# Kernel tuning notes

Measured on AMD Instinct MI355X. Metric: run time of the kernel, lower is better.

## Reference

```python
import jax, jax.numpy as jnp
import numpy as np

HEADS = 8
HEAD_DIM = 32
PRE_H = 32
PRE_W = 32
SCALE = HEAD_DIM ** (-0.5)


def _relative_indices(H, W):
    # Faithful to torch loop: out[p, q] = (gy[q]-y_p+H)*W + (gx[q]-x_p+W)
    gy, gx = np.meshgrid(np.arange(H), np.arange(W), indexing='ij')
    gy = gy.reshape(-1)
    gx = gx.reshape(-1)
    idx = (gy[None, :] - gy[:, None] + H) * W + (gx[None, :] - gx[:, None] + W)
    return idx.astype(np.int32)  # [HW, HW]


def setup_inputs() -> dict:
    key = jax.random.key(0)
    ks = jax.random.split(key, 7)
    b, c, H, W = 16, 256, PRE_H, PRE_W
    dim = HEADS * HEAD_DIM  # 256
    x = jax.random.normal(ks[0], (b, c, H, W), dtype=jnp.float32)
    # nn.Linear weights: [out_features, in_features]
    Wq = jax.random.normal(ks[1], (dim, c), dtype=jnp.float32) * 0.02
    Wk = jax.random.normal(ks[2], (dim, c), dtype=jnp.float32) * 0.02
    Wv = jax.random.normal(ks[3], (dim, c), dtype=jnp.float32) * 0.02
    Wo = jax.random.normal(ks[4], (c, dim), dtype=jnp.float32) * 0.02
    bo = jax.random.normal(ks[5], (c,), dtype=jnp.float32) * 0.02
    rel_bias = jax.random.normal(ks[6], (HEADS, (2 * PRE_H - 1) * (2 * PRE_W - 1)), dtype=jnp.float32)
    rel_idx = jnp.asarray(_relative_indices(PRE_H, PRE_W))
    return {"x": x, "Wq": Wq, "Wk": Wk, "Wv": Wv, "Wo": Wo, "bo": bo,
            "rel_bias": rel_bias, "rel_idx": rel_idx}


def reference(x, Wq, Wk, Wv, Wo, bo, rel_bias, rel_idx):
    b, c, H, W = x.shape
    n = H * W
    h, d = HEADS, HEAD_DIM
    # b c h w -> b (h w) c
    xt = x.reshape(b, c, n).transpose(0, 2, 1)
    q = (xt @ Wq.T).reshape(b, n, h, d).transpose(0, 2, 1, 3)  # b h n d
    k = (xt @ Wk.T).reshape(b, n, h, d).transpose(0, 2, 1, 3)
    v = (xt @ Wv.T).reshape(b, n, h, d).transpose(0, 2, 1, 3)
    k = k * SCALE
    # gathered relative bias: [h, n, n]
    bias = rel_bias[:, rel_idx]
    attn = jnp.einsum('bhnd,bhmd->bhnm', q, k) + bias[None]
    attn = jax.nn.softmax(attn, axis=-1)
    out = jnp.einsum('bhnm,bhmd->bhnd', attn, v)
    out = out.transpose(0, 2, 1, 3).reshape(b, n, h * d)  # b n (h d)
    out = out @ Wo.T + bo
    # b (h w) c -> b c h w
    return out.transpose(0, 2, 1).reshape(b, c, H, W)
```

## Files before the change

### kernel.cpp

```cpp
#include <hip/hip_runtime.h>

#define HEADS 8
#define HDIM 32
#define NTOK 1024
#define CDIM 256
#define BATCH 16
#define ATT_SCALE 0.17677669529663687f
#define L2E 1.4426950408889634f
#define VSTR 1032

typedef __attribute__((ext_vector_type(8))) short bf16x8;
typedef __attribute__((ext_vector_type(4))) float f32x4;

__device__ __forceinline__ unsigned short f2bf(float f) {
    unsigned int u = __float_as_uint(f);
    return (unsigned short)((u + 0x7fffu + ((u >> 16) & 1u)) >> 16);
}

__global__ __launch_bounds__(256) void prep_kernel(
    const float* __restrict__ x,
    const float* __restrict__ Wq, const float* __restrict__ Wk,
    const float* __restrict__ Wv, const float* __restrict__ Wo,
    unsigned short* __restrict__ w16, unsigned short* __restrict__ xt16)
{
    const int t = threadIdx.x;
    if (blockIdx.z == 16) {
        const int which = blockIdx.y;
        const float* src = (which == 0) ? Wq : ((which == 1) ? Wk : ((which == 2) ? Wv : Wo));
        const float scale = (which == 1) ? (ATT_SCALE * L2E) : 1.0f;
        const int base = (blockIdx.x * 256 + t) * 16;
        #pragma unroll
        for (int i = 0; i < 4; ++i) {
            const int idx = base + i * 4;
            float4 v = *(const float4*)&src[idx];
            union { unsigned short h[4]; uint2 u; } pk;
            pk.h[0] = f2bf(v.x * scale); pk.h[1] = f2bf(v.y * scale);
            pk.h[2] = f2bf(v.z * scale); pk.h[3] = f2bf(v.w * scale);
            *(uint2*)&w16[(size_t)which * 65536 + idx] = pk.u;
        }
        return;
    }
    __shared__ float tile[64][65];
    const int b = blockIdx.z, ct = blockIdx.y * 64, nt = blockIdx.x * 64;
    const float* xb = x + ((size_t)b * CDIM + ct) * NTOK + nt;
    const int cc = t >> 4, n4 = (t & 15) * 4;
    #pragma unroll
    for (int i = 0; i < 4; ++i) {
        float4 v = *(const float4*)&xb[(size_t)(cc + 16 * i) * NTOK + n4];
        tile[cc + 16 * i][n4]     = v.x;
        tile[cc + 16 * i][n4 + 1] = v.y;
        tile[cc + 16 * i][n4 + 2] = v.z;
        tile[cc + 16 * i][n4 + 3] = v.w;
    }
    __syncthreads();
    const int c0 = (t & 15) * 4;
    #pragma unroll
    for (int i = 0; i < 4; ++i) {
        const int nl = (t >> 4) + 16 * i;
        union { unsigned short h[4]; uint2 u; } pk;
        #pragma unroll
        for (int j = 0; j < 4; ++j) pk.h[j] = f2bf(tile[c0 + j][nl]);
        *(uint2*)&xt16[((size_t)b * NTOK + nt + nl) * CDIM + ct + c0] = pk.u;
    }
}

__global__ __launch_bounds__(1024, 4) void attn_kernel(
    const unsigned short* __restrict__ xt16,
    const unsigned short* __restrict__ w16,
    const float* __restrict__ rel_bias,
    unsigned short* __restrict__ ao16)
{
    __shared__ __align__(16) unsigned char smem[65536 + VSTR * 32 * 2 + 2080 * 4];
    unsigned short* k_s  = (unsigned short*)smem;
    unsigned short* v_s  = (unsigned short*)(smem + 65536);
    unsigned short* q_s  = (unsigned short*)(smem + 65536);
    float*          bias_s = (float*)(smem + 65536 + VSTR * 32 * 2);

    const int id   = blockIdx.x;
    const int bh_i = (id & 7) * 16 + (id >> 4);
    const int half = (id >> 3) & 1;
    const int b = bh_i >> 3, h = bh_i & 7;

    const int t = threadIdx.x, wid = t >> 6, lane = t & 63;
    const int g = lane >> 4, ln = lane & 15;
    const int qb = half * 512 + wid * 32;

    const unsigned short* xb  = xt16 + (size_t)b * NTOK * CDIM;
    const unsigned short* wqh = w16 + (size_t)(h * 32) * CDIM;
    const unsigned short* wkh = w16 + 65536 + (size_t)(h * 32) * CDIM;
    const unsigned short* wvh = w16 + 2 * 65536 + (size_t)(h * 32) * CDIM;

    {
        const float* brow = rel_bias + (size_t)h * 3969;
        for (int i = t; i < 2080; i += 1024) bias_s[i] = brow[i] * L2E;
    }

    {
        const int tr = wid * 64;
        f32x4 acc[4][2];
        #pragma unroll
        for (int m = 0; m < 4; ++m)
            #pragma unroll
            for (int n = 0; n < 2; ++n) acc[m][n] = (f32x4){0.f, 0.f, 0.f, 0.f};
        for (int kt = 0; kt < CDIM; kt += 32) {
            bf16x8 a[4], w2[2];
            #pragma unroll
            for (int m = 0; m < 4; ++m)
                a[m] = *(const bf16x8*)&xb[(size_t)(tr + m * 16 + ln) * CDIM + kt + g * 8];
            #pragma unroll
            for (int n = 0; n < 2; ++n)
                w2[n] = *(const bf16x8*)&wkh[(size_t)(n * 16 + ln) * CDIM + kt + g * 8];
            #pragma unroll
            for (int m = 0; m < 4; ++m)
                #pragma unroll
                for (int n = 0; n < 2; ++n)
                    acc[m][n] = __builtin_amdgcn_mfma_f32_16x16x32_bf16(a[m], w2[n], acc[m][n], 0, 0, 0);
        }
        #pragma unroll
        for (int m = 0; m < 4; ++m)
            #pragma unroll
            for (int n = 0; n < 2; ++n)
                #pragma unroll
                for (int r = 0; r < 4; ++r)
                    k_s[(size_t)(tr + m * 16 + g * 4 + r) * HDIM + n * 16 + ln] = f2bf(acc[m][n][r]);
    }

    bf16x8 aq0, aq1;
    {
        f32x4 acc[2][2];
        #pragma unroll
        for (int m = 0; m < 2; ++m)
            #pragma unroll
            for (int n = 0; n < 2; ++n) acc[m][n] = (f32x4){0.f, 0.f, 0.f, 0.f};
        for (int kt = 0; kt < CDIM; kt += 32) {
            bf16x8 a[2], w2[2];
            #pragma unroll
            for (int m = 0; m < 2; ++m)
                a[m] = *(const bf16x8*)&xb[(size_t)(qb + m * 16 + ln) * CDIM + kt + g * 8];
            #pragma unroll
            for (int n = 0; n < 2; ++n)
                w2[n] = *(const bf16x8*)&wqh[(size_t)(n * 16 + ln) * CDIM + kt + g * 8];
            #pragma unroll
            for (int m = 0; m < 2; ++m)
                #pragma unroll
                for (int n = 0; n < 2; ++n)
                    acc[m][n] = __builtin_amdgcn_mfma_f32_16x16x32_bf16(a[m], w2[n], acc[m][n], 0, 0, 0);
        }
        const int lr = wid * 32;
        #pragma unroll
        for (int m = 0; m < 2; ++m)
            #pragma unroll
            for (int n = 0; n < 2; ++n)
                #pragma unroll
                for (int r = 0; r < 4; ++r)
                    q_s[(size_t)(lr + m * 16 + g * 4 + r) * HDIM + n * 16 + ln] = f2bf(acc[m][n][r]);
        aq0 = *(const bf16x8*)&q_s[(size_t)(lr + ln) * HDIM + g * 8];
        aq1 = *(const bf16x8*)&q_s[(size_t)(lr + 16 + ln) * HDIM + g * 8];
    }

    __syncthreads();

    {
        const int tb = wid * 64;
        f32x4 acc[2][4];
        #pragma unroll
        for (int m = 0; m < 2; ++m)
            #pragma unroll
            for (int n = 0; n < 4; ++n) acc[m][n] = (f32x4){0.f, 0.f, 0.f, 0.f};
        for (int kt = 0; kt < CDIM; kt += 32) {
            bf16x8 aw[2], bx[4];
            #pragma unroll
            for (int m = 0; m < 2; ++m)
                aw[m] = *(const bf16x8*)&wvh[(size_t)(m * 16 + ln) * CDIM + kt + g * 8];
            #pragma unroll
            for (int n = 0; n < 4; ++n)
                bx[n] = *(const bf16x8*)&xb[(size_t)(tb + n * 16 + ln) * CDIM + kt + g * 8];
            #pragma unroll
            for (int m = 0; m < 2; ++m)
                #pragma unroll
                for (int n = 0; n < 4; ++n)
                    acc[m][n] = __builtin_amdgcn_mfma_f32_16x16x32_bf16(aw[m], bx[n], acc[m][n], 0, 0, 0);
        }
        #pragma unroll
        for (int m = 0; m < 2; ++m)
            #pragma unroll
            for (int n = 0; n < 4; ++n)
                #pragma unroll
                for (int r = 0; r < 4; ++r)
                    v_s[(size_t)(m * 16 + g * 4 + r) * VSTR + tb + n * 16 + ln] = f2bf(acc[m][n][r]);
    }

    __syncthreads();

    const int jrow  = 8 * (ln >> 2) + (ln & 3);
    const int boff0 = 1056 + 8 * g - qb - ln;
    const int boff1 = boff0 - 16;

    f32x4 o00 = {0.f,0.f,0.f,0.f}, o01 = {0.f,0.f,0.f,0.f};
    f32x4 o10 = {0.f,0.f,0.f,0.f}, o11 = {0.f,0.f,0.f,0.f};
    f32x4 ls0 = {0.f,0.f,0.f,0.f}, ls1 = {0.f,0.f,0.f,0.f};
    const short one_bf = (short)0x3F80;
    const bf16x8 ones = {one_bf,one_bf,one_bf,one_bf,one_bf,one_bf,one_bf,one_bf};

    for (int kb = 0; kb < NTOK; kb += 32) {
        const bf16x8 kf0 = *(const bf16x8*)&k_s[(size_t)(kb + jrow) * HDIM + g * 8];
        const bf16x8 kf1 = *(const bf16x8*)&k_s[(size_t)(kb + jrow + 4) * HDIM + g * 8];
        const bf16x8 vA0 = *(const bf16x8*)&v_s[(size_t)ln * VSTR + kb + g * 8];
        const bf16x8 vA1 = *(const bf16x8*)&v_s[(size_t)(16 + ln) * VSTR + kb + g * 8];
        float bc0[8], bc1[8];
        #pragma unroll
        for (int i = 0; i < 8; ++i) bc0[i] = bias_s[kb + boff0 + i];
        #pragma unroll
        for (int i = 0; i < 8; ++i) bc1[i] = bias_s[kb + boff1 + i];

        f32x4 s00 = __builtin_amdgcn_mfma_f32_16x16x32_bf16(kf0, aq0, (f32x4){0.f,0.f,0.f,0.f}, 0, 0, 0);
        f32x4 s01 = __builtin_amdgcn_mfma_f32_16x16x32_bf16(kf1, aq0, (f32x4){0.f,0.f,0.f,0.f}, 0, 0, 0);
        f32x4 s10 = __builtin_amdgcn_mfma_f32_16x16x32_bf16(kf0, aq1, (f32x4){0.f,0.f,0.f,0.f}, 0, 0, 0);
        f32x4 s11 = __builtin_amdgcn_mfma_f32_16x16x32_bf16(kf1, aq1, (f32x4){0.f,0.f,0.f,0.f}, 0, 0, 0);

        union { int i4[4]; bf16x8 v; } ap0, ap1;
        #pragma unroll
        for (int r = 0; r < 4; ++r) {
            float e0 = __builtin_amdgcn_exp2f(s00[r] + bc0[r]);
            float e1 = __builtin_amdgcn_exp2f(s01[r] + bc0[4 + r]);
            unsigned u0 = __float_as_uint(e0) + 0x8000u;
            unsigned u1 = __float_as_uint(e1) + 0x8000u;
            ((unsigned short*)ap0.i4)[r]     = (unsigned short)(u0 >> 16);
            ((unsigned short*)ap0.i4)[4 + r] = (unsigned short)(u1 >> 16);
        }
        #pragma unroll
        for (int r = 0; r < 4; ++r) {
            float e0 = __builtin_amdgcn_exp2f(s10[r] + bc1[r]);
            float e1 = __builtin_amdgcn_exp2f(s11[r] + bc1[4 + r]);
            unsigned u0 = __float_as_uint(e0) + 0x8000u;
            unsigned u1 = __float_as_uint(e1) + 0x8000u;
            ((unsigned short*)ap1.i4)[r]     = (unsigned short)(u0 >> 16);
            ((unsigned short*)ap1.i4)[4 + r] = (unsigned short)(u1 >> 16);
        }

        o00 = __builtin_amdgcn_mfma_f32_16x16x32_bf16(ap0.v, vA0, o00, 0, 0, 0);
        o01 = __builtin_amdgcn_mfma_f32_16x16x32_bf16(ap0.v, vA1, o01, 0, 0, 0);
        ls0 = __builtin_amdgcn_mfma_f32_16x16x32_bf16(ap0.v, ones, ls0, 0, 0, 0);
        o10 = __builtin_amdgcn_mfma_f32_16x16x32_bf16(ap1.v, vA0, o10, 0, 0, 0);
        o11 = __builtin_amdgcn_mfma_f32_16x16x32_bf16(ap1.v, vA1, o11, 0, 0, 0);
        ls1 = __builtin_amdgcn_mfma_f32_16x16x32_bf16(ap1.v, ones, ls1, 0, 0, 0);
    }

    #pragma unroll
    for (int r = 0; r < 4; ++r) {
        float i0 = 1.f / ls0[r], i1 = 1.f / ls1[r];
        o00[r] *= i0; o01[r] *= i0;
        o10[r] *= i1; o11[r] *= i1;
    }

    __syncthreads();
    unsigned short (*otr)[32][40] = (unsigned short(*)[32][40])smem;
    #pragma unroll
    for (int r = 0; r < 4; ++r) {
        otr[wid][g * 4 + r][ln]           = f2bf(o00[r]);
        otr[wid][g * 4 + r][16 + ln]      = f2bf(o01[r]);
        otr[wid][16 + g * 4 + r][ln]      = f2bf(o10[r]);
        otr[wid][16 + g * 4 + r][16 + ln] = f2bf(o11[r]);
    }
    const int row = lane >> 1;
    const int ch  = (lane & 1) * 16;
    uint4 st0 = *(uint4*)&otr[wid][row][ch];
    uint4 st1 = *(uint4*)&otr[wid][row][ch + 8];
    unsigned short* dst = &ao16[((size_t)b * NTOK + qb + row) * CDIM + h * HDIM + ch];
    *(uint4*)dst     = st0;
    *(uint4*)&dst[8] = st1;
}

__global__ __launch_bounds__(256) void outproj_kernel(
    const unsigned short* __restrict__ ao16,
    const unsigned short* __restrict__ wo16,
    const float* __restrict__ bo,
    float* __restrict__ y)
{
    const int id   = blockIdx.x;
    const int b    = (id & 7) * 2 + ((id >> 3) & 1);
    const int rest = id >> 4;
    const int ct   = (rest & 3) * 64;
    const int pt   = (rest >> 2) * 64;
    const int t = threadIdx.x, wid = t >> 6, lane = t & 63;
    const int g = lane >> 4, ln = lane & 15;
    const int cbase = ct + wid * 16;
    const unsigned short* ab = ao16 + (size_t)b * NTOK * CDIM;
    f32x4 acc[4];
    #pragma unroll
    for (int i = 0; i < 4; ++i) acc[i] = (f32x4){0.f, 0.f, 0.f, 0.f};

    for (int kt = 0; kt < CDIM; kt += 32) {
        bf16x8 aw = *(const bf16x8*)&wo16[(size_t)(cbase + ln) * CDIM + kt + g * 8];
        #pragma unroll
        for (int t2 = 0; t2 < 4; ++t2) {
            bf16x8 bx = *(const bf16x8*)&ab[(size_t)(pt + t2 * 16 + ln) * CDIM + kt + g * 8];
            acc[t2] = __builtin_amdgcn_mfma_f32_16x16x32_bf16(aw, bx, acc[t2], 0, 0, 0);
        }
    }
    #pragma unroll
    for (int r = 0; r < 4; ++r) {
        const int c = cbase + g * 4 + r;
        const float bias = bo[c];
        #pragma unroll
        for (int t2 = 0; t2 < 4; ++t2)
            y[((size_t)b * CDIM + c) * NTOK + pt + t2 * 16 + ln] = acc[t2][r] + bias;
    }
}

extern "C" void kernel_launch(void* const* d_in, const int* in_sizes, int n_in,
                              void* d_out, int out_size, void* d_ws, size_t ws_size,
                              hipStream_t stream) {
    const float* x        = (const float*)d_in[0];
    const float* Wq       = (const float*)d_in[1];
    const float* Wk       = (const float*)d_in[2];
    const float* Wv       = (const float*)d_in[3];
    const float* Wo       = (const float*)d_in[4];
    const float* bo       = (const float*)d_in[5];
    const float* rel_bias = (const float*)d_in[6];
    (void)in_sizes; (void)n_in; (void)ws_size; (void)out_size;

    unsigned short* ws16 = (unsigned short*)d_ws;
    unsigned short* xt16 = ws16;
    unsigned short* ao16 = ws16 + (size_t)4 * 1024 * 1024;
    unsigned short* w16  = ws16 + (size_t)8 * 1024 * 1024;
    float* y = (float*)d_out;

    prep_kernel<<<dim3(16, 4, 17), 256, 0, stream>>>(x, Wq, Wk, Wv, Wo, w16, xt16);
    attn_kernel<<<256, 1024, 0, stream>>>(xt16, w16, rel_bias, ao16);
    outproj_kernel<<<1024, 256, 0, stream>>>(ao16, w16 + 3 * 65536, bo, y);
}
```

Measured before the change: 189.3 us.

## Fuse K/V projections, swizzle K smem, seed scores with bias, retile outproj

Computes the K and V projections in one loop so each x fragment is loaded once for both. The K tile in shared memory gets an XOR swizzle to reduce bank conflicts. The relative bias is stored as four shifted copies, so each lane loads it as aligned float4 vectors and feeds it as the MFMA accumulator init, which removes the separate bias adds. The exp-to-bf16 packing is simplified, and the output projection is retiled to 128-token blocks with 2x4 MFMA tiles per wave, halving the grid. Costs are more shared memory for the bias copies and higher register pressure from the fused accumulators and full unrolling.

```diff
diff --git a/kernel.cpp b/kernel.cpp
--- a/kernel.cpp
+++ b/kernel.cpp
@@ -8,6 +8,7 @@
 #define ATT_SCALE 0.17677669529663687f
 #define L2E 1.4426950408889634f
 #define VSTR 1032
+#define BSTR 1540
 
 typedef __attribute__((ext_vector_type(8))) short bf16x8;
 typedef __attribute__((ext_vector_type(4))) float f32x4;
@@ -16,6 +17,8 @@
     unsigned int u = __float_as_uint(f);
     return (unsigned short)((u + 0x7fffu + ((u >> 16) & 1u)) >> 16);
 }
+
+__device__ __forceinline__ int kswz(int row) { return (row + (row >> 3)) & 3; }
 
 __global__ __launch_bounds__(256) void prep_kernel(
     const float* __restrict__ x,
@@ -70,11 +73,11 @@
     const float* __restrict__ rel_bias,
     unsigned short* __restrict__ ao16)
 {
-    __shared__ __align__(16) unsigned char smem[65536 + VSTR * 32 * 2 + 2080 * 4];
-    unsigned short* k_s  = (unsigned short*)smem;
-    unsigned short* v_s  = (unsigned short*)(smem + 65536);
-    unsigned short* q_s  = (unsigned short*)(smem + 65536);
-    float*          bias_s = (float*)(smem + 65536 + VSTR * 32 * 2);
+    __shared__ __align__(16) unsigned char smem[65536 + VSTR * 32 * 2 + BSTR * 4 * 4];
+    unsigned short* k_s   = (unsigned short*)smem;
+    unsigned short* v_s   = (unsigned short*)(smem + 65536);
+    unsigned short* q_s   = (unsigned short*)(smem + 65536);
+    float*          bias4 = (float*)(smem + 65536 + VSTR * 32 * 2);
 
     const int id   = blockIdx.x;
     const int bh_i = (id & 7) * 16 + (id >> 4);
@@ -91,38 +94,13 @@
     const unsigned short* wvh = w16 + 2 * 65536 + (size_t)(h * 32) * CDIM;
 
     {
+        const int START = 544 - 512 * half;
         const float* brow = rel_bias + (size_t)h * 3969;
-        for (int i = t; i < 2080; i += 1024) bias_s[i] = brow[i] * L2E;
-    }
-
-    {
-        const int tr = wid * 64;
-        f32x4 acc[4][2];
-        #pragma unroll
-        for (int m = 0; m < 4; ++m)
-            #pragma unroll
-            for (int n = 0; n < 2; ++n) acc[m][n] = (f32x4){0.f, 0.f, 0.f, 0.f};
-        for (int kt = 0; kt < CDIM; kt += 32) {
-            bf16x8 a[4], w2[2];
-            #pragma unroll
-            for (int m = 0; m < 4; ++m)
-                a[m] = *(const bf16x8*)&xb[(size_t)(tr + m * 16 + ln) * CDIM + kt + g * 8];
-            #pragma unroll
-            for (int n = 0; n < 2; ++n)
-                w2[n] = *(const bf16x8*)&wkh[(size_t)(n * 16 + ln) * CDIM + kt + g * 8];
-            #pragma unroll
-            for (int m = 0; m < 4; ++m)
-                #pragma unroll
-                for (int n = 0; n < 2; ++n)
-                    acc[m][n] = __builtin_amdgcn_mfma_f32_16x16x32_bf16(a[m], w2[n], acc[m][n], 0, 0, 0);
-        }
-        #pragma unroll
-        for (int m = 0; m < 4; ++m)
-            #pragma unroll
-            for (int n = 0; n < 2; ++n)
-                #pragma unroll
-                for (int r = 0; r < 4; ++r)
-                    k_s[(size_t)(tr + m * 16 + g * 4 + r) * HDIM + n * 16 + ln] = f2bf(acc[m][n][r]);
+        for (int i = t; i < 1540; i += 1024) {
+            #pragma unroll
+            for (int a = 0; a < 4; ++a)
+                bias4[a * BSTR + i] = brow[START + a + i] * L2E;
+        }
     }
 
     bf16x8 aq0, aq1;
@@ -132,6 +110,7 @@
         for (int m = 0; m < 2; ++m)
             #pragma unroll
             for (int n = 0; n < 2; ++n) acc[m][n] = (f32x4){0.f, 0.f, 0.f, 0.f};
+        #pragma unroll
         for (int kt = 0; kt < CDIM; kt += 32) {
             bf16x8 a[2], w2[2];
             #pragma unroll
@@ -161,40 +140,64 @@
     __syncthreads();
 
     {
-        const int tb = wid * 64;
-        f32x4 acc[2][4];
-        #pragma unroll
-        for (int m = 0; m < 2; ++m)
-            #pragma unroll
-            for (int n = 0; n < 4; ++n) acc[m][n] = (f32x4){0.f, 0.f, 0.f, 0.f};
+        const int tr = wid * 64;
+        f32x4 ak[4][2], av[2][4];
+        #pragma unroll
+        for (int m = 0; m < 4; ++m)
+            #pragma unroll
+            for (int n = 0; n < 2; ++n) {
+                ak[m][n] = (f32x4){0.f, 0.f, 0.f, 0.f};
+                av[n][m] = (f32x4){0.f, 0.f, 0.f, 0.f};
+            }
+        #pragma unroll
         for (int kt = 0; kt < CDIM; kt += 32) {
-            bf16x8 aw[2], bx[4];
-            #pragma unroll
-            for (int m = 0; m < 2; ++m)
-                aw[m] = *(const bf16x8*)&wvh[(size_t)(m * 16 + ln) * CDIM + kt + g * 8];
-            #pragma unroll
-            for (int n = 0; n < 4; ++n)
-                bx[n] = *(const bf16x8*)&xb[(size_t)(tb + n * 16 + ln) * CDIM + kt + g * 8];
-            #pragma unroll
-            for (int m = 0; m < 2; ++m)
+            bf16x8 xf[4], wkf[2], wvf[2];
+            #pragma unroll
+            for (int m = 0; m < 4; ++m)
+                xf[m] = *(const bf16x8*)&xb[(size_t)(tr + m * 16 + ln) * CDIM + kt + g * 8];
+            #pragma unroll
+            for (int n = 0; n < 2; ++n) {
+                wkf[n] = *(const bf16x8*)&wkh[(size_t)(n * 16 + ln) * CDIM + kt + g * 8];
+                wvf[n] = *(const bf16x8*)&wvh[(size_t)(n * 16 + ln) * CDIM + kt + g * 8];
+            }
+            #pragma unroll
+            for (int m = 0; m < 4; ++m) {
+                ak[m][0] = __builtin_amdgcn_mfma_f32_16x16x32_bf16(xf[m], wkf[0], ak[m][0], 0, 0, 0);
+                ak[m][1] = __builtin_amdgcn_mfma_f32_16x16x32_bf16(xf[m], wkf[1], ak[m][1], 0, 0, 0);
+                av[0][m] = __builtin_amdgcn_mfma_f32_16x16x32_bf16(wvf[0], xf[m], av[0][m], 0, 0, 0);
+                av[1][m] = __builtin_amdgcn_mfma_f32_16x16x32_bf16(wvf[1], xf[m], av[1][m], 0, 0, 0);
+            }
+        }
+        #pragma unroll
+        for (int m = 0; m < 4; ++m)
+            #pragma unroll
+            for (int n = 0; n < 2; ++n)
                 #pragma unroll
-                for (int n = 0; n < 4; ++n)
-                    acc[m][n] = __builtin_amdgcn_mfma_f32_16x16x32_bf16(aw[m], bx[n], acc[m][n], 0, 0, 0);
-        }
-        #pragma unroll
-        for (int m = 0; m < 2; ++m)
-            #pragma unroll
-            for (int n = 0; n < 4; ++n)
+                for (int r = 0; r < 4; ++r) {
+                    const int row = tr + m * 16 + g * 4 + r;
+                    const int col = n * 16 + ln;
+                    k_s[row * 32 + (((col >> 3) ^ kswz(row)) << 3) + (col & 7)] = f2bf(ak[m][n][r]);
+                }
+        #pragma unroll
+        for (int n = 0; n < 2; ++n)
+            #pragma unroll
+            for (int m = 0; m < 4; ++m)
                 #pragma unroll
                 for (int r = 0; r < 4; ++r)
-                    v_s[(size_t)(m * 16 + g * 4 + r) * VSTR + tb + n * 16 + ln] = f2bf(acc[m][n][r]);
+                    v_s[(size_t)(n * 16 + g * 4 + r) * VSTR + tr + m * 16 + ln] = f2bf(av[n][m][r]);
     }
 
     __syncthreads();
 
-    const int jrow  = 8 * (ln >> 2) + (ln & 3);
-    const int boff0 = 1056 + 8 * g - qb - ln;
-    const int boff1 = boff0 - 16;
+    const int jrow = 8 * (ln >> 2) + (ln & 3);
+    const int jr1  = jrow + 4;
+    const int koff0 = jrow * 32 + ((g ^ kswz(jrow)) << 3);
+    const int koff1 = jr1 * 32 + ((g ^ kswz(jr1)) << 3);
+    const int boffL = 512 + 8 * g - wid * 32 - ln;
+    const int ba = boffL & 3;
+    const float* bb = &bias4[ba * BSTR + (boffL - ba)];
+    const unsigned short* vr0 = &v_s[(size_t)ln * VSTR + g * 8];
+    const unsigned short* vr1 = &v_s[(size_t)(16 + ln) * VSTR + g * 8];
 
     f32x4 o00 = {0.f,0.f,0.f,0.f}, o01 = {0.f,0.f,0.f,0.f};
     f32x4 o10 = {0.f,0.f,0.f,0.f}, o11 = {0.f,0.f,0.f,0.f};
@@ -203,39 +206,38 @@
     const bf16x8 ones = {one_bf,one_bf,one_bf,one_bf,one_bf,one_bf,one_bf,one_bf};
 
     for (int kb = 0; kb < NTOK; kb += 32) {
-        const bf16x8 kf0 = *(const bf16x8*)&k_s[(size_t)(kb + jrow) * HDIM + g * 8];
-        const bf16x8 kf1 = *(const bf16x8*)&k_s[(size_t)(kb + jrow + 4) * HDIM + g * 8];
-        const bf16x8 vA0 = *(const bf16x8*)&v_s[(size_t)ln * VSTR + kb + g * 8];
-        const bf16x8 vA1 = *(const bf16x8*)&v_s[(size_t)(16 + ln) * VSTR + kb + g * 8];
-        float bc0[8], bc1[8];
-        #pragma unroll
-        for (int i = 0; i < 8; ++i) bc0[i] = bias_s[kb + boff0 + i];
-        #pragma unroll
-        for (int i = 0; i < 8; ++i) bc1[i] = bias_s[kb + boff1 + i];
-
-        f32x4 s00 = __builtin_amdgcn_mfma_f32_16x16x32_bf16(kf0, aq0, (f32x4){0.f,0.f,0.f,0.f}, 0, 0, 0);
-        f32x4 s01 = __builtin_amdgcn_mfma_f32_16x16x32_bf16(kf1, aq0, (f32x4){0.f,0.f,0.f,0.f}, 0, 0, 0);
-        f32x4 s10 = __builtin_amdgcn_mfma_f32_16x16x32_bf16(kf0, aq1, (f32x4){0.f,0.f,0.f,0.f}, 0, 0, 0);
-        f32x4 s11 = __builtin_amdgcn_mfma_f32_16x16x32_bf16(kf1, aq1, (f32x4){0.f,0.f,0.f,0.f}, 0, 0, 0);
-
-        union { int i4[4]; bf16x8 v; } ap0, ap1;
-        #pragma unroll
-        for (int r = 0; r < 4; ++r) {
-            float e0 = __builtin_amdgcn_exp2f(s00[r] + bc0[r]);
-            float e1 = __builtin_amdgcn_exp2f(s01[r] + bc0[4 + r]);
-            unsigned u0 = __float_as_uint(e0) + 0x8000u;
-            unsigned u1 = __float_as_uint(e1) + 0x8000u;
-            ((unsigned short*)ap0.i4)[r]     = (unsigned short)(u0 >> 16);
-            ((unsigned short*)ap0.i4)[4 + r] = (unsigned short)(u1 >> 16);
-        }
-        #pragma unroll
-        for (int r = 0; r < 4; ++r) {
-            float e0 = __builtin_amdgcn_exp2f(s10[r] + bc1[r]);
-            float e1 = __builtin_amdgcn_exp2f(s11[r] + bc1[4 + r]);
-            unsigned u0 = __float_as_uint(e0) + 0x8000u;
-            unsigned u1 = __float_as_uint(e1) + 0x8000u;
-            ((unsigned short*)ap1.i4)[r]     = (unsigned short)(u0 >> 16);
-            ((unsigned short*)ap1.i4)[4 + r] = (unsigned short)(u1 >> 16);
+        const bf16x8 kf0 = *(const bf16x8*)&k_s[kb * 32 + koff0];
+        const bf16x8 kf1 = *(const bf16x8*)&k_s[kb * 32 + koff1];
+        const bf16x8 vA0 = *(const bf16x8*)&vr0[kb];
+        const bf16x8 vA1 = *(const bf16x8*)&vr1[kb];
+        const f32x4 cA0 = *(const f32x4*)&bb[kb];
+        const f32x4 cA1 = *(const f32x4*)&bb[kb + 4];
+        const f32x4 cB0 = *(const f32x4*)&bb[kb - 16];
+        const f32x4 cB1 = *(const f32x4*)&bb[kb - 12];
+
+        f32x4 s00 = __builtin_amdgcn_mfma_f32_16x16x32_bf16(kf0, aq0, cA0, 0, 0, 0);
+        f32x4 s01 = __builtin_amdgcn_mfma_f32_16x16x32_bf16(kf1, aq0, cA1, 0, 0, 0);
+        f32x4 s10 = __builtin_amdgcn_mfma_f32_16x16x32_bf16(kf0, aq1, cB0, 0, 0, 0);
+        f32x4 s11 = __builtin_amdgcn_mfma_f32_16x16x32_bf16(kf1, aq1, cB1, 0, 0, 0);
+
+        union { unsigned u4[4]; bf16x8 v; } ap0, ap1;
+        #pragma unroll
+        for (int p2 = 0; p2 < 2; ++p2) {
+            unsigned ua = __float_as_uint(__builtin_amdgcn_exp2f(s00[2 * p2]))     + 0x8000u;
+            unsigned ub = __float_as_uint(__builtin_amdgcn_exp2f(s00[2 * p2 + 1])) + 0x8000u;
+            ap0.u4[p2]     = (ub & 0xffff0000u) | (ua >> 16);
+            unsigned uc = __float_as_uint(__builtin_amdgcn_exp2f(s01[2 * p2]))     + 0x8000u;
+            unsigned ud = __float_as_uint(__builtin_amdgcn_exp2f(s01[2 * p2 + 1])) + 0x8000u;
+            ap0.u4[2 + p2] = (ud & 0xffff0000u) | (uc >> 16);
+        }
+        #pragma unroll
+        for (int p2 = 0; p2 < 2; ++p2) {
+            unsigned ua = __float_as_uint(__builtin_amdgcn_exp2f(s10[2 * p2]))     + 0x8000u;
+            unsigned ub = __float_as_uint(__builtin_amdgcn_exp2f(s10[2 * p2 + 1])) + 0x8000u;
+            ap1.u4[p2]     = (ub & 0xffff0000u) | (ua >> 16);
+            unsigned uc = __float_as_uint(__builtin_amdgcn_exp2f(s11[2 * p2]))     + 0x8000u;
+            unsigned ud = __float_as_uint(__builtin_amdgcn_exp2f(s11[2 * p2 + 1])) + 0x8000u;
+            ap1.u4[2 + p2] = (ud & 0xffff0000u) | (uc >> 16);
         }
 
         o00 = __builtin_amdgcn_mfma_f32_16x16x32_bf16(ap0.v, vA0, o00, 0, 0, 0);
@@ -281,31 +283,44 @@
     const int b    = (id & 7) * 2 + ((id >> 3) & 1);
     const int rest = id >> 4;
     const int ct   = (rest & 3) * 64;
-    const int pt   = (rest >> 2) * 64;
+    const int pt   = (rest >> 2) * 128;
     const int t = threadIdx.x, wid = t >> 6, lane = t & 63;
     const int g = lane >> 4, ln = lane & 15;
-    const int cbase = ct + wid * 16;
+    const int cb2 = ct + (wid & 1) * 32;
+    const int pb  = pt + (wid >> 1) * 64;
     const unsigned short* ab = ao16 + (size_t)b * NTOK * CDIM;
-    f32x4 acc[4];
-    #pragma unroll
-    for (int i = 0; i < 4; ++i) acc[i] = (f32x4){0.f, 0.f, 0.f, 0.f};
-
+
+    f32x4 acc[2][4];
+    #pragma unroll
+    for (int n = 0; n < 2; ++n)
+        #pragma unroll
+        for (int m = 0; m < 4; ++m) acc[n][m] = (f32x4){0.f, 0.f, 0.f, 0.f};
+
+    #pragma unroll
     for (int kt = 0; kt < CDIM; kt += 32) {
-        bf16x8 aw = *(const bf16x8*)&wo16[(size_t)(cbase + ln) * CDIM + kt + g * 8];
-        #pragma unroll
-        for (int t2 = 0; t2 < 4; ++t2) {
-            bf16x8 bx = *(const bf16x8*)&ab[(size_t)(pt + t2 * 16 + ln) * CDIM + kt + g * 8];
-            acc[t2] = __builtin_amdgcn_mfma_f32_16x16x32_bf16(aw, bx, acc[t2], 0, 0, 0);
-        }
-    }
-    #pragma unroll
-    for (int r = 0; r < 4; ++r) {
-        const int c = cbase + g * 4 + r;
-        const float bias = bo[c];
-        #pragma unroll
-        for (int t2 = 0; t2 < 4; ++t2)
-            y[((size_t)b * CDIM + c) * NTOK + pt + t2 * 16 + ln] = acc[t2][r] + bias;
-    }
+        bf16x8 aw[2], bx[4];
+        #pragma unroll
+        for (int n = 0; n < 2; ++n)
+            aw[n] = *(const bf16x8*)&wo16[(size_t)(cb2 + n * 16 + ln) * CDIM + kt + g * 8];
+        #pragma unroll
+        for (int m = 0; m < 4; ++m)
+            bx[m] = *(const bf16x8*)&ab[(size_t)(pb + m * 16 + ln) * CDIM + kt + g * 8];
+        #pragma unroll
+        for (int n = 0; n < 2; ++n)
+            #pragma unroll
+            for (int m = 0; m < 4; ++m)
+                acc[n][m] = __builtin_amdgcn_mfma_f32_16x16x32_bf16(aw[n], bx[m], acc[n][m], 0, 0, 0);
+    }
+    #pragma unroll
+    for (int n = 0; n < 2; ++n)
+        #pragma unroll
+        for (int r = 0; r < 4; ++r) {
+            const int c = cb2 + n * 16 + g * 4 + r;
+            const float bias = bo[c];
+            #pragma unroll
+            for (int m = 0; m < 4; ++m)
+                y[((size_t)b * CDIM + c) * NTOK + pb + m * 16 + ln] = acc[n][m][r] + bias;
+        }
 }
 
 extern "C" void kernel_launch(void* const* d_in, const int* in_sizes, int n_in,
@@ -328,5 +343,5 @@
 
     prep_kernel<<<dim3(16, 4, 17), 256, 0, stream>>>(x, Wq, Wk, Wv, Wo, w16, xt16);
     attn_kernel<<<256, 1024, 0, stream>>>(xt16, w16, rel_bias, ao16);
-    outproj_kernel<<<1024, 256, 0, stream>>>(ao16, w16 + 3 * 65536, bo, y);
-}
+    outproj_kernel<<<512, 256, 0, stream>>>(ao16, w16 + 3 * 65536, bo, y);
+}
```

Measured after the change: 172.7 us. 8.8% less time.
